# Kernel optimization log

Hardware: AMD Instinct MI355X
Metric: run time of the kernel (lower is better)

The kernel has to match this reference:

```python
import jax, jax.numpy as jnp
import numpy as np

N, E, CIN, COUT, T = 50000, 800000, 64, 64, 12


def setup_inputs() -> dict:
    key = jax.random.key(0)
    k1, k2, k3, k4, k5, k6 = jax.random.split(key, 6)
    x = jax.random.normal(k1, (N, CIN, T), dtype=jnp.float32)
    src = jax.random.randint(k2, (E,), 0, N, dtype=jnp.int32)
    dst = jax.random.randint(k3, (E,), 0, N, dtype=jnp.int32)
    edge_index = jnp.stack([src, dst], axis=0)
    edge_attr = jax.random.uniform(k4, (E,), dtype=jnp.float32)
    W = jax.random.normal(k5, (CIN, COUT), dtype=jnp.float32) / np.sqrt(CIN)
    b = jax.random.normal(k6, (COUT,), dtype=jnp.float32) * 0.01
    return {"x": x, "edge_index": edge_index, "edge_attr": edge_attr, "W": W, "b": b}


def reference(x, edge_index, edge_attr, W, b):
    # GCNConv applied independently to each of T temporal slices, then ReLU.
    n = x.shape[0]
    src, dst = edge_index[0], edge_index[1]
    # add self-loops with weight 1.0 (PyG GCNConv default)
    loop = jnp.arange(n, dtype=src.dtype)
    src_f = jnp.concatenate([src, loop])
    dst_f = jnp.concatenate([dst, loop])
    ew = jnp.concatenate([edge_attr, jnp.ones((n,), x.dtype)])
    # symmetric normalization: deg computed at target (col) nodes
    deg = jax.ops.segment_sum(ew, dst_f, num_segments=n)
    dis = jnp.where(deg > 0, jax.lax.rsqrt(deg), 0.0)
    norm = dis[src_f] * ew * dis[dst_f]  # (E+N,)

    def step(carry, x_t):  # x_t: (N, Cin)
        xw = x_t @ W                              # (N, Cout)
        msgs = xw[src_f] * norm[:, None]          # (E+N, Cout) gather
        out = jax.ops.segment_sum(msgs, dst_f, num_segments=n) + b
        return carry, jax.nn.relu(out)

    _, ys = jax.lax.scan(step, None, jnp.transpose(x, (2, 0, 1)))  # (T, N, Cout)
    return jnp.transpose(ys, (1, 2, 0))  # (N, Cout, T)
```

## Files before the change

kernel.cpp:

```cpp
#include <hip/hip_runtime.h>

#define CIN   64
#define COUT  64
#define TT    12
#define FEAT  (CIN * TT)
#define QROW  (FEAT / 4)

typedef unsigned int uint32;
typedef unsigned long long u64;
typedef float  __attribute__((ext_vector_type(4))) f32x4;

#define DEG_SCALE 1048576.0f

__global__ __launch_bounds__(256) void k_cvt_deg(
    const f32x4* __restrict__ x, uint2* __restrict__ xh, int nquads, int nbCvt,
    const int* __restrict__ dst, const float* __restrict__ ea,
    u64* __restrict__ deg64, int e_cnt)
{
    int bid = blockIdx.x;
    if (bid < nbCvt) {
        int i = bid * 256 + threadIdx.x;
        int stride = nbCvt * 256;
        for (; i < nquads; i += stride) {
            f32x4 v = __builtin_nontemporal_load(&x[i]);
            uint32 u0 = __float_as_uint(v.x), u1 = __float_as_uint(v.y);
            uint32 u2 = __float_as_uint(v.z), u3 = __float_as_uint(v.w);
            u0 = (u0 + 0x7fffu + ((u0 >> 16) & 1)) >> 16;
            u1 = (u1 + 0x7fffu + ((u1 >> 16) & 1)) >> 16;
            u2 = (u2 + 0x7fffu + ((u2 >> 16) & 1)) >> 16;
            u3 = (u3 + 0x7fffu + ((u3 >> 16) & 1)) >> 16;
            uint2 o; o.x = u0 | (u1 << 16); o.y = u2 | (u3 << 16);
            xh[i] = o;
        }
    } else {
        int e = (bid - nbCvt) * 256 + threadIdx.x;
        if (e < e_cnt) {
            u64 v = ((u64)1 << 32) | (u64)(uint32)(ea[e] * DEG_SCALE + 0.5f);
            atomicAdd(&deg64[dst[e]], v);
        }
    }
}

__global__ __launch_bounds__(256) void k_disred(const u64* __restrict__ deg64,
                                                float* __restrict__ dis,
                                                int* __restrict__ partial, int n) {
    __shared__ int red[256];
    int t = threadIdx.x;
    int i = blockIdx.x * 256 + t;
    int cnt = 0;
    if (i < n) {
        u64 v = deg64[i];
        cnt = (int)(v >> 32);
        float deg = 1.0f + (float)(uint32)v * (1.0f / DEG_SCALE);
        dis[i] = rsqrtf(deg);
    }
    red[t] = cnt;
    __syncthreads();
    for (int off = 128; off > 0; off >>= 1) {
        if (t < off) red[t] += red[t + off];
        __syncthreads();
    }
    if (t == 0) partial[blockIdx.x] = red[0];
}

__global__ __launch_bounds__(256) void k_scanwrite(const u64* __restrict__ deg64,
                                                   const int* __restrict__ partial,
                                                   int nb,
                                                   int* __restrict__ rowptr,
                                                   int* __restrict__ cursor, int n) {
    __shared__ int tmp[256];
    __shared__ int pred[256];
    int t = threadIdx.x;
    int bid = blockIdx.x;
    int i = bid * 256 + t;

    int pv = (t < nb) ? partial[t] : 0;
    pred[t] = (t < bid) ? pv : 0;
    int v = (i < n) ? (int)(deg64[i] >> 32) : 0;
    tmp[t] = v;
    __syncthreads();
    for (int off = 128; off > 0; off >>= 1) {
        if (t < off) pred[t] += pred[t + off];
        __syncthreads();
    }
    for (int off = 1; off < 256; off <<= 1) {
        int u = (t >= off) ? tmp[t - off] : 0;
        __syncthreads();
        tmp[t] += u;
        __syncthreads();
    }
    int blockOff = pred[0];
    int excl = tmp[t] - v + blockOff;
    if (i < n) { rowptr[i] = excl; cursor[i] = excl; }
    if (bid == nb - 1 && t == 255) rowptr[n] = blockOff + tmp[255];
}

__global__ void k_fill(const int* __restrict__ src, const int* __restrict__ dst,
                       const float* __restrict__ ea, const float* __restrict__ dis,
                       int* __restrict__ cursor, int2* __restrict__ csr, int e_cnt) {
    int e = blockIdx.x * blockDim.x + threadIdx.x;
    if (e < e_cnt) {
        int s = src[e], d = dst[e];
        int pos = atomicAdd(&cursor[d], 1);
        float w = dis[s] * ea[e] * dis[d];
        int2 p; p.x = s; p.y = __float_as_int(w);
        csr[pos] = p;
    }
}

template <int BF16>
__global__ __launch_bounds__(192) void k_conv(
    const void* __restrict__ xsrc, const float* __restrict__ W,
    const float* __restrict__ b, const float* __restrict__ dis,
    const int* __restrict__ rowptr, const int2* __restrict__ csr,
    float* __restrict__ out)
{
    __shared__ float sAgg[FEAT];
    __shared__ int2  sE[192];
    __shared__ float sB[COUT];

    const int n = blockIdx.x;
    const int t = threadIdx.x;
    if (t < COUT) sB[t] = b[t];

    const int start = rowptr[n];
    const int end   = rowptr[n + 1];
    const float dn  = dis[n];
    const float selfw = dn * dn;

    float a0, a1, a2, a3;
    if (BF16) {
        const uint2* xb = (const uint2*)xsrc;
        uint2 v = xb[(size_t)n * QROW + t];
        a0 = selfw * __uint_as_float(v.x << 16);
        a1 = selfw * __uint_as_float(v.x & 0xffff0000u);
        a2 = selfw * __uint_as_float(v.y << 16);
        a3 = selfw * __uint_as_float(v.y & 0xffff0000u);
    } else {
        const f32x4* xb = (const f32x4*)xsrc;
        f32x4 v = xb[(size_t)n * QROW + t];
        a0 = selfw * v.x; a1 = selfw * v.y; a2 = selfw * v.z; a3 = selfw * v.w;
    }

    for (int base = start; base < end; base += 192) {
        int cnt = end - base; if (cnt > 192) cnt = 192;
        __syncthreads();
        if (t < cnt) sE[t] = csr[base + t];
        __syncthreads();
        for (int j = 0; j < cnt; ++j) {
            int s    = sE[j].x;
            float w  = __int_as_float(sE[j].y);
            if (BF16) {
                const uint2* xb = (const uint2*)xsrc;
                uint2 v = xb[(size_t)s * QROW + t];
                a0 = fmaf(w, __uint_as_float(v.x << 16),         a0);
                a1 = fmaf(w, __uint_as_float(v.x & 0xffff0000u), a1);
                a2 = fmaf(w, __uint_as_float(v.y << 16),         a2);
                a3 = fmaf(w, __uint_as_float(v.y & 0xffff0000u), a3);
            } else {
                const f32x4* xb = (const f32x4*)xsrc;
                f32x4 v = xb[(size_t)s * QROW + t];
                a0 = fmaf(w, v.x, a0); a1 = fmaf(w, v.y, a1);
                a2 = fmaf(w, v.z, a2); a3 = fmaf(w, v.w, a3);
            }
        }
    }

    float4 av; av.x = a0; av.y = a1; av.z = a2; av.w = a3;
    *((float4*)&sAgg[4 * t]) = av;
    __syncthreads();

    const int co  = t & 63;
    const int tg  = t >> 6;
    const int tt0 = tg * 4;
    float o0 = sB[co], o1 = o0, o2 = o0, o3 = o0;
#pragma unroll
    for (int c = 0; c < CIN; ++c) {
        float wv = W[c * COUT + co];
        o0 = fmaf(wv, sAgg[c * TT + tt0    ], o0);
        o1 = fmaf(wv, sAgg[c * TT + tt0 + 1], o1);
        o2 = fmaf(wv, sAgg[c * TT + tt0 + 2], o2);
        o3 = fmaf(wv, sAgg[c * TT + tt0 + 3], o3);
    }
    o0 = fmaxf(o0, 0.0f); o1 = fmaxf(o1, 0.0f);
    o2 = fmaxf(o2, 0.0f); o3 = fmaxf(o3, 0.0f);

    __syncthreads();
    float4 ov; ov.x = o0; ov.y = o1; ov.z = o2; ov.w = o3;
    *((float4*)&sAgg[co * TT + tt0]) = ov;
    __syncthreads();
    f32x4 r = *((const f32x4*)&sAgg[4 * t]);
    __builtin_nontemporal_store(r, (f32x4*)(out + (size_t)n * FEAT + 4 * t));
}

extern "C" void kernel_launch(void* const* d_in, const int* in_sizes, int n_in,
                              void* d_out, int out_size, void* d_ws, size_t ws_size,
                              hipStream_t stream) {
    const float* x   = (const float*)d_in[0];
    const int*   ei  = (const int*)d_in[1];
    const float* ea  = (const float*)d_in[2];
    const float* W   = (const float*)d_in[3];
    const float* b   = (const float*)d_in[4];
    float* out = (float*)d_out;

    const int E = in_sizes[2];
    const int N = in_sizes[0] / FEAT;
    const int* src = ei;
    const int* dst = ei + E;

    size_t off = 0;
    char* ws = (char*)d_ws;
    auto alloc = [&](size_t bytes) -> char* {
        char* p = ws + off;
        off = (off + bytes + 15) & ~(size_t)15;
        return p;
    };
    u64*   deg64   = (u64*)  alloc((size_t)N * 8);
    float* dis     = (float*)alloc((size_t)N * 4);
    int*   rowptr  = (int*)  alloc((size_t)(N + 1) * 4);
    int*   cursor  = (int*)  alloc((size_t)N * 4);
    int*   partial = (int*)  alloc(4096);
    int2*  csr     = (int2*) alloc((size_t)E * 8);
    unsigned short* xh = (unsigned short*)alloc((size_t)N * FEAT * 2);
    const bool use_bf16 = (off <= ws_size);

    int nb_e = (E + 255) / 256;
    int nb_n = (N + 255) / 256;

    (void)hipMemsetAsync(deg64, 0, (size_t)N * 8, stream);
    if (use_bf16) {
        int nquads = (N * FEAT) / 4;
        int nbCvt = 1024;
        k_cvt_deg<<<nbCvt + nb_e, 256, 0, stream>>>((const f32x4*)x, (uint2*)xh,
                                                    nquads, nbCvt, dst, ea, deg64, E);
    } else {
        k_cvt_deg<<<nb_e, 256, 0, stream>>>(nullptr, nullptr, 0, 0, dst, ea, deg64, E);
    }
    k_disred   <<<nb_n, 256, 0, stream>>>(deg64, dis, partial, N);
    k_scanwrite<<<nb_n, 256, 0, stream>>>(deg64, partial, nb_n, rowptr, cursor, N);
    k_fill     <<<nb_e, 256, 0, stream>>>(src, dst, ea, dis, cursor, csr, E);
    if (use_bf16)
        k_conv<1><<<N, 192, 0, stream>>>(xh, W, b, dis, rowptr, csr, out);
    else
        k_conv<0><<<N, 192, 0, stream>>>(x,  W, b, dis, rowptr, csr, out);
}
```

Before: 326.7 us.

## Fuse CSR setup kernels into one cooperative kernel with grid syncs

Replaces the memset plus four setup kernels (convert/degree, dis-reduce, scan, fill) with one cooperative kernel of 1024 blocks that separates the phases with grid.sync(). This removes several launch gaps and the memset. In exchange, the degree atomics no longer overlap the bf16 conversion, which now runs to completion first, and the grid-wide barriers add their own cost. The scan phase assumes nb_n (196) fits within the 1024 resident blocks.

```diff
diff --git a/kernel.cpp b/kernel.cpp
--- a/kernel.cpp
+++ b/kernel.cpp
@@ -1,4 +1,7 @@
 #include <hip/hip_runtime.h>
+#include <hip/hip_cooperative_groups.h>
+
+namespace cg = cooperative_groups;
 
 #define CIN   64
 #define COUT  64
@@ -12,16 +15,24 @@
 
 #define DEG_SCALE 1048576.0f
 
-__global__ __launch_bounds__(256) void k_cvt_deg(
-    const f32x4* __restrict__ x, uint2* __restrict__ xh, int nquads, int nbCvt,
-    const int* __restrict__ dst, const float* __restrict__ ea,
-    u64* __restrict__ deg64, int e_cnt)
+__global__ __launch_bounds__(256, 4) void k_setup(
+    const f32x4* __restrict__ x, uint2* __restrict__ xh, int nquads,
+    const int* __restrict__ src, const int* __restrict__ dst,
+    const float* __restrict__ ea,
+    u64* __restrict__ deg64, float* __restrict__ dis,
+    int* __restrict__ rowptr, int* __restrict__ cursor,
+    int* __restrict__ partial, int2* __restrict__ csr,
+    int N, int E, int nb_n)
 {
-    int bid = blockIdx.x;
-    if (bid < nbCvt) {
-        int i = bid * 256 + threadIdx.x;
-        int stride = nbCvt * 256;
-        for (; i < nquads; i += stride) {
+    cg::grid_group grid = cg::this_grid();
+    const int t    = threadIdx.x;
+    const int bid  = blockIdx.x;
+    const int gtid = bid * 256 + t;
+    const int gsz  = gridDim.x * 256;
+
+    for (int i = gtid; i < N; i += gsz) deg64[i] = 0;
+    if (xh != nullptr) {
+        for (int i = gtid; i < nquads; i += gsz) {
             f32x4 v = __builtin_nontemporal_load(&x[i]);
             uint32 u0 = __float_as_uint(v.x), u1 = __float_as_uint(v.y);
             uint32 u2 = __float_as_uint(v.z), u3 = __float_as_uint(v.w);
@@ -32,74 +43,60 @@
             uint2 o; o.x = u0 | (u1 << 16); o.y = u2 | (u3 << 16);
             xh[i] = o;
         }
-    } else {
-        int e = (bid - nbCvt) * 256 + threadIdx.x;
-        if (e < e_cnt) {
-            u64 v = ((u64)1 << 32) | (u64)(uint32)(ea[e] * DEG_SCALE + 0.5f);
-            atomicAdd(&deg64[dst[e]], v);
-        }
-    }
-}
-
-__global__ __launch_bounds__(256) void k_disred(const u64* __restrict__ deg64,
-                                                float* __restrict__ dis,
-                                                int* __restrict__ partial, int n) {
+    }
+    grid.sync();
+
+    for (int e = gtid; e < E; e += gsz) {
+        u64 v = ((u64)1 << 32) | (u64)(uint32)(ea[e] * DEG_SCALE + 0.5f);
+        atomicAdd(&deg64[dst[e]], v);
+    }
+    grid.sync();
+
     __shared__ int red[256];
-    int t = threadIdx.x;
-    int i = blockIdx.x * 256 + t;
-    int cnt = 0;
-    if (i < n) {
-        u64 v = deg64[i];
-        cnt = (int)(v >> 32);
-        float deg = 1.0f + (float)(uint32)v * (1.0f / DEG_SCALE);
-        dis[i] = rsqrtf(deg);
-    }
-    red[t] = cnt;
-    __syncthreads();
-    for (int off = 128; off > 0; off >>= 1) {
-        if (t < off) red[t] += red[t + off];
-        __syncthreads();
-    }
-    if (t == 0) partial[blockIdx.x] = red[0];
-}
-
-__global__ __launch_bounds__(256) void k_scanwrite(const u64* __restrict__ deg64,
-                                                   const int* __restrict__ partial,
-                                                   int nb,
-                                                   int* __restrict__ rowptr,
-                                                   int* __restrict__ cursor, int n) {
+    if (bid < nb_n) {
+        int i = bid * 256 + t;
+        int cnt = 0;
+        if (i < N) {
+            u64 v = deg64[i];
+            cnt = (int)(v >> 32);
+            dis[i] = rsqrtf(1.0f + (float)(uint32)v * (1.0f / DEG_SCALE));
+        }
+        red[t] = cnt;
+        __syncthreads();
+        for (int off = 128; off > 0; off >>= 1) {
+            if (t < off) red[t] += red[t + off];
+            __syncthreads();
+        }
+        if (t == 0) partial[bid] = red[0];
+    }
+    grid.sync();
+
     __shared__ int tmp[256];
     __shared__ int pred[256];
-    int t = threadIdx.x;
-    int bid = blockIdx.x;
-    int i = bid * 256 + t;
-
-    int pv = (t < nb) ? partial[t] : 0;
-    pred[t] = (t < bid) ? pv : 0;
-    int v = (i < n) ? (int)(deg64[i] >> 32) : 0;
-    tmp[t] = v;
-    __syncthreads();
-    for (int off = 128; off > 0; off >>= 1) {
-        if (t < off) pred[t] += pred[t + off];
-        __syncthreads();
-    }
-    for (int off = 1; off < 256; off <<= 1) {
-        int u = (t >= off) ? tmp[t - off] : 0;
-        __syncthreads();
-        tmp[t] += u;
-        __syncthreads();
-    }
-    int blockOff = pred[0];
-    int excl = tmp[t] - v + blockOff;
-    if (i < n) { rowptr[i] = excl; cursor[i] = excl; }
-    if (bid == nb - 1 && t == 255) rowptr[n] = blockOff + tmp[255];
-}
-
-__global__ void k_fill(const int* __restrict__ src, const int* __restrict__ dst,
-                       const float* __restrict__ ea, const float* __restrict__ dis,
-                       int* __restrict__ cursor, int2* __restrict__ csr, int e_cnt) {
-    int e = blockIdx.x * blockDim.x + threadIdx.x;
-    if (e < e_cnt) {
+    if (bid < nb_n) {
+        int i = bid * 256 + t;
+        int pv = (t < nb_n) ? partial[t] : 0;
+        pred[t] = (t < bid) ? pv : 0;
+        int v = (i < N) ? (int)(deg64[i] >> 32) : 0;
+        tmp[t] = v;
+        __syncthreads();
+        for (int off = 128; off > 0; off >>= 1) {
+            if (t < off) pred[t] += pred[t + off];
+            __syncthreads();
+        }
+        for (int off = 1; off < 256; off <<= 1) {
+            int u = (t >= off) ? tmp[t - off] : 0;
+            __syncthreads();
+            tmp[t] += u;
+            __syncthreads();
+        }
+        int excl = tmp[t] - v + pred[0];
+        if (i < N) { rowptr[i] = excl; cursor[i] = excl; }
+        if (bid == nb_n - 1 && t == 255) rowptr[N] = pred[0] + tmp[255];
+    }
+    grid.sync();
+
+    for (int e = gtid; e < E; e += gsz) {
         int s = src[e], d = dst[e];
         int pos = atomicAdd(&cursor[d], 1);
         float w = dis[s] * ea[e] * dis[d];
@@ -224,21 +221,27 @@
     unsigned short* xh = (unsigned short*)alloc((size_t)N * FEAT * 2);
     const bool use_bf16 = (off <= ws_size);
 
-    int nb_e = (E + 255) / 256;
-    int nb_n = (N + 255) / 256;
-
-    (void)hipMemsetAsync(deg64, 0, (size_t)N * 8, stream);
-    if (use_bf16) {
-        int nquads = (N * FEAT) / 4;
-        int nbCvt = 1024;
-        k_cvt_deg<<<nbCvt + nb_e, 256, 0, stream>>>((const f32x4*)x, (uint2*)xh,
-                                                    nquads, nbCvt, dst, ea, deg64, E);
-    } else {
-        k_cvt_deg<<<nb_e, 256, 0, stream>>>(nullptr, nullptr, 0, 0, dst, ea, deg64, E);
-    }
-    k_disred   <<<nb_n, 256, 0, stream>>>(deg64, dis, partial, N);
-    k_scanwrite<<<nb_n, 256, 0, stream>>>(deg64, partial, nb_n, rowptr, cursor, N);
-    k_fill     <<<nb_e, 256, 0, stream>>>(src, dst, ea, dis, cursor, csr, E);
+    int nb_n   = (N + 255) / 256;
+    int nquads = (N * FEAT) / 4;
+
+    {
+        const f32x4* xp = (const f32x4*)x;
+        uint2* xhp = use_bf16 ? (uint2*)xh : nullptr;
+        const int* srcp = src; const int* dstp = dst;
+        const float* eap = ea;
+        int Nv = N, Ev = E, nbv = nb_n, nq = nquads;
+        void* params[] = {
+            (void*)&xp, (void*)&xhp, (void*)&nq,
+            (void*)&srcp, (void*)&dstp, (void*)&eap,
+            (void*)&deg64, (void*)&dis, (void*)&rowptr, (void*)&cursor,
+            (void*)&partial, (void*)&csr,
+            (void*)&Nv, (void*)&Ev, (void*)&nbv
+        };
+        (void)hipLaunchCooperativeKernel((const void*)k_setup,
+                                         dim3(1024), dim3(256),
+                                         params, 0, stream);
+    }
+
     if (use_bf16)
         k_conv<1><<<N, 192, 0, stream>>>(xh, W, b, dis, rowptr, csr, out);
     else
```

Result: slower. 732.3 us (+124.1%).

## Apply weight GEMM before aggregation and gather bf16 XW rows

Applied to the files above, without the earlier changes.

The dense transform x·W now happens first, fused into the bf16 conversion/degree kernel, so the per-node conv kernel only gathers precomputed XW rows, then adds bias, applies ReLU and stores. This removes the per-block shared-memory GEMM and the W reads from the conv kernel, which ran once per node. It moves that GEMM into a grid-strided kernel that stages W in LDS and processes two nodes per block. Rounding now happens after the matmul rather than on the raw inputs, which slightly changes numerics.

```diff
diff --git a/kernel.cpp b/kernel.cpp
--- a/kernel.cpp
+++ b/kernel.cpp
@@ -12,28 +12,54 @@
 
 #define DEG_SCALE 1048576.0f
 
-__global__ __launch_bounds__(256) void k_cvt_deg(
-    const f32x4* __restrict__ x, uint2* __restrict__ xh, int nquads, int nbCvt,
+__global__ __launch_bounds__(384) void k_ygemm_deg(
+    const float* __restrict__ x, const float* __restrict__ W,
+    unsigned short* __restrict__ yh, int Nnodes, int nbY,
     const int* __restrict__ dst, const float* __restrict__ ea,
     u64* __restrict__ deg64, int e_cnt)
 {
-    int bid = blockIdx.x;
-    if (bid < nbCvt) {
-        int i = bid * 256 + threadIdx.x;
-        int stride = nbCvt * 256;
-        for (; i < nquads; i += stride) {
-            f32x4 v = __builtin_nontemporal_load(&x[i]);
-            uint32 u0 = __float_as_uint(v.x), u1 = __float_as_uint(v.y);
-            uint32 u2 = __float_as_uint(v.z), u3 = __float_as_uint(v.w);
-            u0 = (u0 + 0x7fffu + ((u0 >> 16) & 1)) >> 16;
-            u1 = (u1 + 0x7fffu + ((u1 >> 16) & 1)) >> 16;
-            u2 = (u2 + 0x7fffu + ((u2 >> 16) & 1)) >> 16;
-            u3 = (u3 + 0x7fffu + ((u3 >> 16) & 1)) >> 16;
-            uint2 o; o.x = u0 | (u1 << 16); o.y = u2 | (u3 << 16);
-            xh[i] = o;
+    const int bid = blockIdx.x;
+    const int t   = threadIdx.x;
+    if (bid < nbY) {
+        __shared__ float sW[CIN * COUT];
+        __shared__ float sx[2][FEAT];
+        for (int i = t; i < CIN * COUT; i += 384) sW[i] = W[i];
+        const int sub = t / 192;
+        const int tl  = t - sub * 192;
+        const int co  = tl / 3;
+        const int ttg = tl - co * 3;
+        const int tb  = ttg * 4;
+        __syncthreads();
+        for (int n0 = bid * 2; n0 < Nnodes; n0 += nbY * 2) {
+            int n = n0 + sub;
+            if (n < Nnodes) {
+                const f32x4* xr = (const f32x4*)(x + (size_t)n * FEAT);
+                *((f32x4*)&sx[sub][tl * 4]) = xr[tl];
+            }
+            __syncthreads();
+            if (n < Nnodes) {
+                float o0 = 0, o1 = 0, o2 = 0, o3 = 0;
+#pragma unroll
+                for (int c = 0; c < CIN; ++c) {
+                    float wv = sW[c * COUT + co];
+                    o0 = fmaf(wv, sx[sub][c * TT + tb    ], o0);
+                    o1 = fmaf(wv, sx[sub][c * TT + tb + 1], o1);
+                    o2 = fmaf(wv, sx[sub][c * TT + tb + 2], o2);
+                    o3 = fmaf(wv, sx[sub][c * TT + tb + 3], o3);
+                }
+                uint32 u0 = __float_as_uint(o0), u1 = __float_as_uint(o1);
+                uint32 u2 = __float_as_uint(o2), u3 = __float_as_uint(o3);
+                u0 = (u0 + 0x7fffu + ((u0 >> 16) & 1)) >> 16;
+                u1 = (u1 + 0x7fffu + ((u1 >> 16) & 1)) >> 16;
+                u2 = (u2 + 0x7fffu + ((u2 >> 16) & 1)) >> 16;
+                u3 = (u3 + 0x7fffu + ((u3 >> 16) & 1)) >> 16;
+                uint2 o; o.x = u0 | (u1 << 16); o.y = u2 | (u3 << 16);
+                ((uint2*)(yh + (size_t)n * FEAT))[co * 3 + ttg] = o;
+            }
+            __syncthreads();
         }
     } else {
-        int e = (bid - nbCvt) * 256 + threadIdx.x;
+        int e = (bid - nbY) * 384 + t;
         if (e < e_cnt) {
             u64 v = ((u64)1 << 32) | (u64)(uint32)(ea[e] * DEG_SCALE + 0.5f);
             atomicAdd(&deg64[dst[e]], v);
@@ -51,8 +77,7 @@
     if (i < n) {
         u64 v = deg64[i];
         cnt = (int)(v >> 32);
-        float deg = 1.0f + (float)(uint32)v * (1.0f / DEG_SCALE);
-        dis[i] = rsqrtf(deg);
+        dis[i] = rsqrtf(1.0f + (float)(uint32)v * (1.0f / DEG_SCALE));
     }
     red[t] = cnt;
     __syncthreads();
@@ -108,9 +133,54 @@
     }
 }
 
-template <int BF16>
-__global__ __launch_bounds__(192) void k_conv(
-    const void* __restrict__ xsrc, const float* __restrict__ W,
+__global__ __launch_bounds__(192) void k_conv_y(
+    const unsigned short* __restrict__ yh, const float* __restrict__ b,
+    const float* __restrict__ dis, const int* __restrict__ rowptr,
+    const int2* __restrict__ csr, float* __restrict__ out)
+{
+    __shared__ int2 sE[192];
+
+    const int n = blockIdx.x;
+    const int t = threadIdx.x;
+    const int start = rowptr[n];
+    const int end   = rowptr[n + 1];
+    const float dn  = dis[n];
+    const float selfw = dn * dn;
+
+    const uint2* yb = (const uint2*)yh;
+    uint2 v = yb[(size_t)n * QROW + t];
+    float a0 = selfw * __uint_as_float(v.x << 16);
+    float a1 = selfw * __uint_as_float(v.x & 0xffff0000u);
+    float a2 = selfw * __uint_as_float(v.y << 16);
+    float a3 = selfw * __uint_as_float(v.y & 0xffff0000u);
+
+    for (int base = start; base < end; base += 192) {
+        int cnt = end - base; if (cnt > 192) cnt = 192;
+        __syncthreads();
+        if (t < cnt) sE[t] = csr[base + t];
+        __syncthreads();
+        for (int j = 0; j < cnt; ++j) {
+            int s    = sE[j].x;
+            float w  = __int_as_float(sE[j].y);
+            uint2 u = yb[(size_t)s * QROW + t];
+            a0 = fmaf(w, __uint_as_float(u.x << 16),         a0);
+            a1 = fmaf(w, __uint_as_float(u.x & 0xffff0000u), a1);
+            a2 = fmaf(w, __uint_as_float(u.y << 16),         a2);
+            a3 = fmaf(w, __uint_as_float(u.y & 0xffff0000u), a3);
+        }
+    }
+
+    const int f = 4 * t;
+    f32x4 r;
+    r.x = fmaxf(a0 + b[ f      / 12], 0.0f);
+    r.y = fmaxf(a1 + b[(f + 1) / 12], 0.0f);
+    r.z = fmaxf(a2 + b[(f + 2) / 12], 0.0f);
+    r.w = fmaxf(a3 + b[(f + 3) / 12], 0.0f);
+    __builtin_nontemporal_store(r, (f32x4*)(out + (size_t)n * FEAT + f));
+}
+
+__global__ __launch_bounds__(192) void k_conv_x(
+    const float* __restrict__ xsrc, const float* __restrict__ W,
     const float* __restrict__ b, const float* __restrict__ dis,
     const int* __restrict__ rowptr, const int2* __restrict__ csr,
     float* __restrict__ out)
@@ -128,19 +198,9 @@
     const float dn  = dis[n];
     const float selfw = dn * dn;
 
-    float a0, a1, a2, a3;
-    if (BF16) {
-        const uint2* xb = (const uint2*)xsrc;
-        uint2 v = xb[(size_t)n * QROW + t];
-        a0 = selfw * __uint_as_float(v.x << 16);
-        a1 = selfw * __uint_as_float(v.x & 0xffff0000u);
-        a2 = selfw * __uint_as_float(v.y << 16);
-        a3 = selfw * __uint_as_float(v.y & 0xffff0000u);
-    } else {
-        const f32x4* xb = (const f32x4*)xsrc;
-        f32x4 v = xb[(size_t)n * QROW + t];
-        a0 = selfw * v.x; a1 = selfw * v.y; a2 = selfw * v.z; a3 = selfw * v.w;
-    }
+    const f32x4* xb = (const f32x4*)xsrc;
+    f32x4 v = xb[(size_t)n * QROW + t];
+    float a0 = selfw * v.x, a1 = selfw * v.y, a2 = selfw * v.z, a3 = selfw * v.w;
 
     for (int base = start; base < end; base += 192) {
         int cnt = end - base; if (cnt > 192) cnt = 192;
@@ -150,19 +210,9 @@
         for (int j = 0; j < cnt; ++j) {
             int s    = sE[j].x;
             float w  = __int_as_float(sE[j].y);
-            if (BF16) {
-                const uint2* xb = (const uint2*)xsrc;
-                uint2 v = xb[(size_t)s * QROW + t];
-                a0 = fmaf(w, __uint_as_float(v.x << 16),         a0);
-                a1 = fmaf(w, __uint_as_float(v.x & 0xffff0000u), a1);
-                a2 = fmaf(w, __uint_as_float(v.y << 16),         a2);
-                a3 = fmaf(w, __uint_as_float(v.y & 0xffff0000u), a3);
-            } else {
-                const f32x4* xb = (const f32x4*)xsrc;
-                f32x4 v = xb[(size_t)s * QROW + t];
-                a0 = fmaf(w, v.x, a0); a1 = fmaf(w, v.y, a1);
-                a2 = fmaf(w, v.z, a2); a3 = fmaf(w, v.w, a3);
-            }
+            f32x4 u = xb[(size_t)s * QROW + t];
+            a0 = fmaf(w, u.x, a0); a1 = fmaf(w, u.y, a1);
+            a2 = fmaf(w, u.z, a2); a3 = fmaf(w, u.w, a3);
         }
     }
 
@@ -221,26 +271,27 @@
     int*   cursor  = (int*)  alloc((size_t)N * 4);
     int*   partial = (int*)  alloc(4096);
     int2*  csr     = (int2*) alloc((size_t)E * 8);
-    unsigned short* xh = (unsigned short*)alloc((size_t)N * FEAT * 2);
+    unsigned short* yh = (unsigned short*)alloc((size_t)N * FEAT * 2);
     const bool use_bf16 = (off <= ws_size);
 
-    int nb_e = (E + 255) / 256;
-    int nb_n = (N + 255) / 256;
+    int nb_n   = (N + 255) / 256;
+    int nb_e   = (E + 255) / 256;
+    int nb_e384 = (E + 383) / 384;
 
     (void)hipMemsetAsync(deg64, 0, (size_t)N * 8, stream);
     if (use_bf16) {
-        int nquads = (N * FEAT) / 4;
-        int nbCvt = 1024;
-        k_cvt_deg<<<nbCvt + nb_e, 256, 0, stream>>>((const f32x4*)x, (uint2*)xh,
-                                                    nquads, nbCvt, dst, ea, deg64, E);
+        int nbY = 1280;
+        k_ygemm_deg<<<nbY + nb_e384, 384, 0, stream>>>(x, W, yh, N, nbY,
+                                                       dst, ea, deg64, E);
     } else {
-        k_cvt_deg<<<nb_e, 256, 0, stream>>>(nullptr, nullptr, 0, 0, dst, ea, deg64, E);
+        k_ygemm_deg<<<nb_e384, 384, 0, stream>>>(x, W, nullptr, N, 0,
+                                                 dst, ea, deg64, E);
     }
     k_disred   <<<nb_n, 256, 0, stream>>>(deg64, dis, partial, N);
     k_scanwrite<<<nb_n, 256, 0, stream>>>(deg64, partial, nb_n, rowptr, cursor, N);
     k_fill     <<<nb_e, 256, 0, stream>>>(src, dst, ea, dis, cursor, csr, E);
     if (use_bf16)
-        k_conv<1><<<N, 192, 0, stream>>>(xh, W, b, dis, rowptr, csr, out);
+        k_conv_y<<<N, 192, 0, stream>>>(yh, b, dis, rowptr, csr, out);
     else
-        k_conv<0><<<N, 192, 0, stream>>>(x,  W, b, dis, rowptr, csr, out);
-}
+        k_conv_x<<<N, 192, 0, stream>>>(x, W, b, dis, rowptr, csr, out);
+}
```

Result: slower. 422.5 us (+29.3%).
